# Kernel tuning notes

Hardware: AMD Instinct MI355X
Metric: run time of the kernel (lower is better)

The kernel has to match this reference:

```python
import jax, jax.numpy as jnp
import numpy as np

B, L, H, E, MODES = 32, 2048, 8, 64, 64
SCALE = 1.0 / (512 * 512)  # 1/(in_channels*out_channels)


def setup_inputs() -> dict:
    key = jax.random.key(0)
    kq, kk, kv, kwr, kwi = jax.random.split(key, 5)
    # frequency mode selection: shuffled range(L//2), first MODES, sorted (get_frequency_modes)
    rng = np.random.default_rng(0)
    index = np.sort(rng.permutation(L // 2)[:MODES]).astype(np.int32)
    return {
        "q": jax.random.normal(kq, (B, L, H, E), dtype=jnp.float32),
        "k": jax.random.normal(kk, (B, L, H, E), dtype=jnp.float32),
        "v": jax.random.normal(kv, (B, L, H, E), dtype=jnp.float32),
        "w_real": SCALE * jax.random.uniform(kwr, (H, E, E, MODES), dtype=jnp.float32),
        "w_imag": SCALE * jax.random.uniform(kwi, (H, E, E, MODES), dtype=jnp.float32),
        "index": jnp.asarray(index),
    }


def reference(q, k, v, w_real, w_imag, index):
    # q: [B, L, H, E]; k, v unused by FourierBlock
    Bq, Lq, Hq, Eq = q.shape
    x = jnp.transpose(q, (0, 2, 3, 1))            # [B, H, E, L]
    x_ft = jnp.fft.rfft(x, axis=-1)               # [B, H, E, L//2+1] complex
    xs = jnp.take(x_ft, index, axis=-1)           # gather selected modes: [B, H, E, M]
    W = w_real + 1j * w_imag                      # [H, E, E, M] complex
    # vectorized per-mode complex einsum ('bhi,hio->bho' over all modes m)
    out = jnp.einsum('bhim,hiom->bhom', xs, W)    # [B, H, E, M]
    n_freq = Lq // 2 + 1
    # original writes mode wi into slot wi (0..M-1), rest stay zero
    out_ft = jnp.concatenate(
        [out, jnp.zeros((Bq, Hq, Eq, n_freq - out.shape[-1]), dtype=out.dtype)], axis=-1)
    return jnp.fft.irfft(out_ft, n=Lq, axis=-1)   # [B, H, E, L] real
```

## Files before the change

kernel.cpp:

```cpp
#include <hip/hip_runtime.h>
#include <math.h>

#define NB 32
#define NL 2048
#define NH 8
#define NE 64
#define NM 64
#define MRI 128

typedef __attribute__((ext_vector_type(8))) __bf16 bf16x8;
typedef __attribute__((ext_vector_type(2))) __bf16 bf16x2;
typedef __attribute__((ext_vector_type(8))) unsigned short us8;
typedef __attribute__((ext_vector_type(4))) float f32x4;
typedef __attribute__((ext_vector_type(16))) float f32x16;

__device__ __forceinline__ unsigned short f2bf(float x) {
  unsigned int u = __builtin_bit_cast(unsigned int, x);
  u = (u + 0x7fffu + ((u >> 16) & 1u)) >> 16;
  return (unsigned short)u;
}
__device__ __forceinline__ float bf2f(unsigned short u) {
  return __builtin_bit_cast(float, (unsigned int)u << 16);
}
__device__ __forceinline__ unsigned int pk2(float lo, float hi) {
  bf16x2 v;
  v[0] = (__bf16)lo;
  v[1] = (__bf16)hi;
  return __builtin_bit_cast(unsigned int, v);
}
__device__ __forceinline__ void gll16(const void* g, void* l) {
  __builtin_amdgcn_global_load_lds(
      (const __attribute__((address_space(1))) void*)g,
      (__attribute__((address_space(3))) void*)l, 16, 0, 0);
}

__global__ void tables_k(const int* __restrict__ idx,
                         const float* __restrict__ wr, const float* __restrict__ wi,
                         unsigned short* __restrict__ T, unsigned short* __restrict__ IT,
                         unsigned short* __restrict__ WBr, unsigned short* __restrict__ WBi) {
  int gid = blockIdx.x * blockDim.x + threadIdx.x;
  const float w0 = 6.283185307179586f / (float)NL;
  {
    int row = gid >> 11, l = gid & (NL - 1);
    int m = row & 63;
    int f = idx[m];
    float s, c;
    sincosf((float)((f * l) & (NL - 1)) * w0, &s, &c);
    T[gid] = f2bf(row < 64 ? c : -s);
  }
  {
    int lp = gid >> 7, k = gid & 127;
    int m = k & 63;
    float s, c;
    sincosf((float)((m * lp) & (NL - 1)) * w0, &s, &c);
    float v = (k < 64) ? ((m == 0 ? 1.0f : 2.0f) / (float)NL) * c
                       : (m == 0 ? 0.0f : (-2.0f / (float)NL) * s);
    IT[gid] = f2bf(v);
  }
  {
    const float2* wr2 = (const float2*)wr;
    const float2* wi2 = (const float2*)wi;
    unsigned int* obr = (unsigned int*)WBr;
    unsigned int* obi = (unsigned int*)WBi;
#pragma unroll
    for (int r = 0; r < 4; ++r) {
      int j = r * 262144 + gid;
      float2 a = wr2[j];
      float2 b2 = wi2[j];
      obr[j] = pk2(a.x, a.y);
      obi[j] = pk2(b2.x, b2.y);
    }
  }
}

__global__ __launch_bounds__(512) void fused_k(const float* __restrict__ q,
                                               const unsigned short* __restrict__ T,
                                               const unsigned short* __restrict__ IT,
                                               const unsigned short* __restrict__ WBr,
                                               const unsigned short* __restrict__ WBi,
                                               float* __restrict__ out) {
  __shared__ __align__(16) char smem[51200];
  int t = threadIdx.x, lane = t & 63, wid = t >> 6;
  int h = blockIdx.x & 7, b = blockIdx.x >> 3;

  {
    unsigned short* Al = (unsigned short*)smem;
    char* Bl = smem + 32768;
    const float* qb = q + ((size_t)b * NL * NH + h) * NE;
    int mh = wid >> 1, eh = wid & 1;
    int ts = t & 255;
    int eq = ts >> 4, lq = ts & 15;
    bool stagerB = (wid < 4);
    f32x4 acc[2][2] = {};
    f32x4 st[4];

    auto stageA = [&](int bufi, int k0) {
      int t2 = t - 256;
#pragma unroll
      for (int n = 0; n < 4; ++n) {
        int lin = n * 4096 + t2 * 16;
        int row = lin >> 7;
        int colb = (lin & 127) ^ ((row & 7) << 4);
        gll16((const char*)T + (size_t)row * (NL * 2) + (size_t)k0 * 2 + colb,
              (char*)Al + bufi * 16384 + lin);
      }
    };
    auto loadsB = [&](int c) {
#pragma unroll
      for (int p = 0; p < 4; ++p)
        st[p] = *(const f32x4*)(qb + (size_t)(c * 64 + lq * 4 + p) * (NH * NE) + eq * 4);
    };
    auto writesB = [&](int bufi) {
      char* base = Bl + bufi * 9216;
#pragma unroll
      for (int j = 0; j < 4; ++j) {
        int e = eq * 4 + j;
        unsigned int w0 = pk2(st[0][j], st[1][j]);
        unsigned int w1 = pk2(st[2][j], st[3][j]);
        *(uint2*)(base + e * 144 + lq * 8) = make_uint2(w0, w1);
      }
    };
    auto compute = [&](int bufi) {
      const char* ab = (const char*)Al + bufi * 16384;
      const char* bb = Bl + bufi * 9216;
#pragma unroll
      for (int ks2 = 0; ks2 < 2; ++ks2) {
        bf16x8 bfr[2];
#pragma unroll
        for (int fn = 0; fn < 2; ++fn) {
          int e = eh * 32 + fn * 16 + (lane & 15);
          bfr[fn] = __builtin_bit_cast(
              bf16x8, *(const us8*)(bb + e * 144 + ks2 * 64 + (lane >> 4) * 16));
        }
#pragma unroll
        for (int fm = 0; fm < 2; ++fm) {
          int row = mh * 32 + fm * 16 + (lane & 15);
          int off = ((row << 7) + (ks2 << 6) + ((lane >> 4) << 4)) ^ ((row & 7) << 4);
          bf16x8 afr = __builtin_bit_cast(bf16x8, *(const us8*)(ab + off));
          acc[fm][0] = __builtin_amdgcn_mfma_f32_16x16x32_bf16(afr, bfr[0], acc[fm][0], 0, 0, 0);
          acc[fm][1] = __builtin_amdgcn_mfma_f32_16x16x32_bf16(afr, bfr[1], acc[fm][1], 0, 0, 0);
        }
      }
    };

    if (stagerB) { loadsB(0); writesB(0); } else { stageA(0, 0); }
    __syncthreads();
    for (int c = 0; c < 32; ++c) {
      int cur = c & 1;
      bool more = (c + 1) < 32;
      if (more) {
        if (stagerB) loadsB(c + 1);
        else stageA(cur ^ 1, (c + 1) * 64);
      }
      compute(cur);
      if (more && stagerB) writesB(cur ^ 1);
      __syncthreads();
    }
#pragma unroll
    for (int fm = 0; fm < 2; ++fm)
#pragma unroll
      for (int fn = 0; fn < 2; ++fn)
#pragma unroll
        for (int r4 = 0; r4 < 4; ++r4) {
          int row = mh * 32 + fm * 16 + (lane >> 4) * 4 + r4;
          int col = eh * 32 + fn * 16 + (lane & 15);
          int off = (row * 272 + col * 4) ^ (((row >> 3) & 7) << 4);
          *(float*)(smem + off) = acc[fm][fn][r4];
        }
  }
  __syncthreads();

  {
    char* OtB = smem + 34816;
    int o = t >> 3, mq = t & 7;
    const unsigned short* wbr = WBr + (size_t)h * 262144 + (size_t)o * 64 + mq * 8;
    const unsigned short* wbi = WBi + (size_t)h * 262144 + (size_t)o * 64 + mq * 8;
    float orr[8] = {}, oii[8] = {};
    for (int ib = 0; ib < 16; ++ib) {
      f32x4 xr4[8], xi4[8];
#pragma unroll
      for (int mi = 0; mi < 8; ++mi) {
        int m = mq * 8 + mi;
        xr4[mi] = *(const f32x4*)(smem + ((m * 272 + ib * 16) ^ (mq << 4)));
        xi4[mi] = *(const f32x4*)(smem + (((64 + m) * 272 + ib * 16) ^ (mq << 4)));
      }
      us8 wr8[4], wi8[4];
#pragma unroll
      for (int ii = 0; ii < 4; ++ii) {
        int i = ib * 4 + ii;
        wr8[ii] = *(const us8*)(wbr + (size_t)i * 4096);
        wi8[ii] = *(const us8*)(wbi + (size_t)i * 4096);
      }
#pragma unroll
      for (int ii = 0; ii < 4; ++ii)
#pragma unroll
        for (int mi = 0; mi < 8; ++mi) {
          float wrv = bf2f(wr8[ii][mi]);
          float wiv = bf2f(wi8[ii][mi]);
          orr[mi] += xr4[mi][ii] * wrv - xi4[mi][ii] * wiv;
          oii[mi] += xr4[mi][ii] * wiv + xi4[mi][ii] * wrv;
        }
    }
    uint4 vr = make_uint4(pk2(orr[0], orr[1]), pk2(orr[2], orr[3]),
                          pk2(orr[4], orr[5]), pk2(orr[6], orr[7]));
    uint4 vi = make_uint4(pk2(oii[0], oii[1]), pk2(oii[2], oii[3]),
                          pk2(oii[4], oii[5]), pk2(oii[6], oii[7]));
    *(uint4*)(OtB + ((o * 256 + mq * 16) ^ ((o & 7) << 4))) = vr;
    *(uint4*)(OtB + ((o * 256 + 128 + mq * 16) ^ ((o & 7) << 4))) = vi;
  }
  __syncthreads();

  {
    const char* OtB = smem + 34816;
    bf16x8 af[2][8];
#pragma unroll
    for (int rg2 = 0; rg2 < 2; ++rg2)
#pragma unroll
      for (int ks = 0; ks < 8; ++ks) {
        int row = rg2 * 32 + (lane & 31);
        int off = (row * 256 + ks * 32 + (lane >> 5) * 16) ^ ((row & 7) << 4);
        af[rg2][ks] = __builtin_bit_cast(bf16x8, *(const us8*)(OtB + off));
      }
    float* ob = out + ((size_t)(b * 8 + h) * 64) * NL;
    int l0 = wid * 256;
    for (int ct = 0; ct < 8; ++ct) {
      int lr = l0 + ct * 32 + (lane & 31);
      f32x16 a2[2] = {};
#pragma unroll
      for (int ks = 0; ks < 8; ++ks) {
        bf16x8 bv = __builtin_bit_cast(
            bf16x8, *(const us8*)(IT + (size_t)lr * MRI + ks * 16 + (lane >> 5) * 8));
        a2[0] = __builtin_amdgcn_mfma_f32_32x32x16_bf16(af[0][ks], bv, a2[0], 0, 0, 0);
        a2[1] = __builtin_amdgcn_mfma_f32_32x32x16_bf16(af[1][ks], bv, a2[1], 0, 0, 0);
      }
#pragma unroll
      for (int rg2 = 0; rg2 < 2; ++rg2)
#pragma unroll
        for (int rg = 0; rg < 16; ++rg) {
          int row = rg2 * 32 + ((rg & 3) + 8 * (rg >> 2) + 4 * (lane >> 5));
          ob[(size_t)row * NL + lr] = a2[rg2][rg];
        }
    }
  }
}

extern "C" void kernel_launch(void* const* d_in, const int* in_sizes, int n_in,
                              void* d_out, int out_size, void* d_ws, size_t ws_size,
                              hipStream_t stream) {
  const float* q = (const float*)d_in[0];
  const float* wr = (const float*)d_in[3];
  const float* wi = (const float*)d_in[4];
  const int* idx = (const int*)d_in[5];
  float* out = (float*)d_out;
  char* ws = (char*)d_ws;

  constexpr size_t TBYTES = (size_t)MRI * NL * 2;
  constexpr size_t WBBYTES = (size_t)NH * NE * NE * NM * 2;
  constexpr size_t NEED = 2 * TBYTES + 2 * WBBYTES;
  if (ws_size < NEED) return;

  unsigned short* T = (unsigned short*)ws;
  unsigned short* IT = (unsigned short*)(ws + TBYTES);
  unsigned short* WBr = (unsigned short*)(ws + 2 * TBYTES);
  unsigned short* WBi = (unsigned short*)(ws + 2 * TBYTES + WBBYTES);

  hipLaunchKernelGGL(tables_k, dim3(1024), dim3(256), 0, stream, idx, wr, wi, T, IT, WBr, WBi);
  hipLaunchKernelGGL(fused_k, dim3(NB * NH), dim3(512), 0, stream, q, T, IT, WBr, WBi, out);
}
```

Measured before the change: 96.35 us.

## Load DFT table fragments directly to registers and pipeline q staging across all waves

The forward-DFT GEMM stage no longer stages the twiddle table through LDS with warp-specialized loader waves. Each wave now loads its A fragments straight from global memory into registers, double-buffered. All 512 threads share the q transpose-and-convert into two ping-pong LDS buffers, synchronised with lgkmcnt waits plus raw barriers. This removes LDS traffic and the producer/consumer imbalance for A, at the cost of uncoalesced-ish global loads for T per wave, more registers, and an extra __syncthreads later because the B buffers now overlap the output staging region.

Result: slower. 109.1 us (+13.2%).

```diff
diff --git a/kernel.cpp b/kernel.cpp
--- a/kernel.cpp
+++ b/kernel.cpp
@@ -28,10 +28,9 @@
   v[1] = (__bf16)hi;
   return __builtin_bit_cast(unsigned int, v);
 }
-__device__ __forceinline__ void gll16(const void* g, void* l) {
-  __builtin_amdgcn_global_load_lds(
-      (const __attribute__((address_space(1))) void*)g,
-      (__attribute__((address_space(3))) void*)l, 16, 0, 0);
+__device__ __forceinline__ void bar_lgkm() {
+  asm volatile("s_waitcnt lgkmcnt(0)" ::: "memory");
+  __builtin_amdgcn_s_barrier();
 }
 
 __global__ void tables_k(const int* __restrict__ idx,
@@ -79,50 +78,44 @@
                                                const unsigned short* __restrict__ WBr,
                                                const unsigned short* __restrict__ WBi,
                                                float* __restrict__ out) {
-  __shared__ __align__(16) char smem[51200];
+  __shared__ __align__(16) char smem[53248];
   int t = threadIdx.x, lane = t & 63, wid = t >> 6;
   int h = blockIdx.x & 7, b = blockIdx.x >> 3;
 
   {
-    unsigned short* Al = (unsigned short*)smem;
-    char* Bl = smem + 32768;
+    char* b0 = smem + 34816;
+    char* b1 = smem + 44032;
     const float* qb = q + ((size_t)b * NL * NH + h) * NE;
     int mh = wid >> 1, eh = wid & 1;
-    int ts = t & 255;
-    int eq = ts >> 4, lq = ts & 15;
-    bool stagerB = (wid < 4);
+    int eq = t >> 5, lp = t & 31;
     f32x4 acc[2][2] = {};
-    f32x4 st[4];
-
-    auto stageA = [&](int bufi, int k0) {
-      int t2 = t - 256;
-#pragma unroll
-      for (int n = 0; n < 4; ++n) {
-        int lin = n * 4096 + t2 * 16;
-        int row = lin >> 7;
-        int colb = (lin & 127) ^ ((row & 7) << 4);
-        gll16((const char*)T + (size_t)row * (NL * 2) + (size_t)k0 * 2 + colb,
-              (char*)Al + bufi * 16384 + lin);
-      }
-    };
-    auto loadsB = [&](int c) {
-#pragma unroll
-      for (int p = 0; p < 4; ++p)
-        st[p] = *(const f32x4*)(qb + (size_t)(c * 64 + lq * 4 + p) * (NH * NE) + eq * 4);
-    };
-    auto writesB = [&](int bufi) {
-      char* base = Bl + bufi * 9216;
+    us8 aregA[4], aregB[4];
+    f32x4 qregA[2], qregB[2];
+
+    auto qload = [&](int c, f32x4* qr) {
+#pragma unroll
+      for (int j2 = 0; j2 < 2; ++j2)
+        qr[j2] = *(const f32x4*)(qb + (size_t)(c * 64 + lp * 2 + j2) * (NH * NE) + eq * 4);
+    };
+    auto writesB = [&](const f32x4* qr, char* bb) {
 #pragma unroll
       for (int j = 0; j < 4; ++j) {
         int e = eq * 4 + j;
-        unsigned int w0 = pk2(st[0][j], st[1][j]);
-        unsigned int w1 = pk2(st[2][j], st[3][j]);
-        *(uint2*)(base + e * 144 + lq * 8) = make_uint2(w0, w1);
-      }
-    };
-    auto compute = [&](int bufi) {
-      const char* ab = (const char*)Al + bufi * 16384;
-      const char* bb = Bl + bufi * 9216;
+        *(unsigned int*)(bb + e * 144 + lp * 4) = pk2(qr[0][j], qr[1][j]);
+      }
+    };
+    auto loadA = [&](int c, us8* ar) {
+#pragma unroll
+      for (int ks2 = 0; ks2 < 2; ++ks2)
+#pragma unroll
+        for (int fm = 0; fm < 2; ++fm) {
+          int row = mh * 32 + fm * 16 + (lane & 15);
+          ar[ks2 * 2 + fm] = *(const us8*)(
+              (const char*)T + (size_t)row * (NL * 2) +
+              (size_t)(c * 64 + ks2 * 32 + (lane >> 4) * 8) * 2);
+        }
+    };
+    auto compute = [&](const us8* ar, const char* bb) {
 #pragma unroll
       for (int ks2 = 0; ks2 < 2; ++ks2) {
         bf16x8 bfr[2];
@@ -134,27 +127,33 @@
         }
 #pragma unroll
         for (int fm = 0; fm < 2; ++fm) {
-          int row = mh * 32 + fm * 16 + (lane & 15);
-          int off = ((row << 7) + (ks2 << 6) + ((lane >> 4) << 4)) ^ ((row & 7) << 4);
-          bf16x8 afr = __builtin_bit_cast(bf16x8, *(const us8*)(ab + off));
+          bf16x8 afr = __builtin_bit_cast(bf16x8, ar[ks2 * 2 + fm]);
           acc[fm][0] = __builtin_amdgcn_mfma_f32_16x16x32_bf16(afr, bfr[0], acc[fm][0], 0, 0, 0);
           acc[fm][1] = __builtin_amdgcn_mfma_f32_16x16x32_bf16(afr, bfr[1], acc[fm][1], 0, 0, 0);
         }
       }
     };
 
-    if (stagerB) { loadsB(0); writesB(0); } else { stageA(0, 0); }
-    __syncthreads();
-    for (int c = 0; c < 32; ++c) {
-      int cur = c & 1;
-      bool more = (c + 1) < 32;
-      if (more) {
-        if (stagerB) loadsB(c + 1);
-        else stageA(cur ^ 1, (c + 1) * 64);
-      }
-      compute(cur);
-      if (more && stagerB) writesB(cur ^ 1);
-      __syncthreads();
+    qload(0, qregA);
+    qload(1, qregB);
+    writesB(qregA, b0);
+    loadA(0, aregA);
+    bar_lgkm();
+    for (int cc = 0; cc < 32; cc += 2) {
+      loadA(cc + 1, aregB);
+      compute(aregA, b0);
+      __builtin_amdgcn_s_barrier();
+      writesB(qregB, b1);
+      if (cc + 2 < 32) qload(cc + 2, qregA);
+      bar_lgkm();
+      if (cc + 2 < 32) loadA(cc + 2, aregA);
+      compute(aregB, b1);
+      __builtin_amdgcn_s_barrier();
+      if (cc + 2 < 32) {
+        writesB(qregA, b0);
+        if (cc + 3 < 32) qload(cc + 3, qregB);
+        bar_lgkm();
+      }
     }
 #pragma unroll
     for (int fm = 0; fm < 2; ++fm)
@@ -201,6 +200,7 @@
           oii[mi] += xr4[mi][ii] * wiv + xi4[mi][ii] * wrv;
         }
     }
+    __syncthreads();
     uint4 vr = make_uint4(pk2(orr[0], orr[1]), pk2(orr[2], orr[3]),
                           pk2(orr[4], orr[5]), pk2(orr[6], orr[7]));
     uint4 vi = make_uint4(pk2(oii[0], oii[1]), pk2(oii[2], oii[3]),
```
